# Kernel tuning notes

Hardware: AMD Instinct MI355X
Metric: run time of the kernel (lower is better)

The kernel has to match this reference:

```python
import jax, jax.numpy as jnp
import numpy as np

EPS = 1e-6

def setup_inputs() -> dict:
    key = jax.random.key(0)
    ks = jax.random.split(key, 9)
    B, T, D = 4, 1024, 128
    sc = 1.0 / np.sqrt(D)
    return {
        "x_seq": jax.random.normal(ks[0], (B, T, D), dtype=jnp.float32),
        "Wq": jax.random.uniform(ks[1], (D, D), jnp.float32, -sc, sc),
        "bq": jax.random.uniform(ks[2], (D,), jnp.float32, -sc, sc),
        "Wk": jax.random.uniform(ks[3], (D, D), jnp.float32, -sc, sc),
        "bk": jax.random.uniform(ks[4], (D,), jnp.float32, -sc, sc),
        "Wv": jax.random.uniform(ks[5], (D, D), jnp.float32, -sc, sc),
        "bv": jax.random.uniform(ks[6], (D,), jnp.float32, -sc, sc),
        "Wa": jax.random.uniform(ks[7], (D, D), jnp.float32, -sc, sc),
        "ba": jax.random.uniform(ks[8], (D,), jnp.float32, -sc, sc),
    }

def reference(x_seq, Wq, bq, Wk, bk, Wv, bv, Wa, ba):
    B, T, D = x_seq.shape
    q = jax.nn.relu(x_seq @ Wq.T + bq)          # [B,T,D]
    k = jax.nn.relu(x_seq @ Wk.T + bk)
    v = x_seq @ Wv.T + bv
    A = jax.nn.sigmoid(x_seq @ Wa.T + ba)       # per-step decay gate

    def step(carry, inp):
        s, z = carry                             # s:[B,D,D], z:[B,D]
        a_t, k_t, v_t, q_t = inp                 # each [B,D]
        s = a_t[:, :, None] * s + k_t[:, :, None] * v_t[:, None, :]  # s[b,i,j]=a_i*s + k_i v_j
        z = a_t * z + k_t
        num = jnp.einsum('bi,bij->bj', q_t, s)
        den = jnp.sum(q_t * z, axis=-1, keepdims=True) + EPS
        return (s, z), num / den

    s0 = jnp.zeros((B, D, D), x_seq.dtype)
    z0 = jnp.zeros((B, D), x_seq.dtype)
    xs = (jnp.swapaxes(A, 0, 1), jnp.swapaxes(k, 0, 1),
          jnp.swapaxes(v, 0, 1), jnp.swapaxes(q, 0, 1))  # time-major [T,B,D]
    _, y = jax.lax.scan(step, (s0, z0), xs)
    return jnp.swapaxes(y, 0, 1)                 # [B,T,D]
```

## Files before the change

kernel.cpp:

```cpp
#include <hip/hip_runtime.h>

#define BB 4
#define TT 1024
#define DD 128
#define LL 32
#define CC 32
#define EPSV 1e-6f

#define BTD (BB*TT*DD)
#define BCD (BB*CC*DD)

#define OFF_QC   0
#define OFF_KH   (OFF_QC + BTD)
#define OFF_V    (OFF_KH + BTD)
#define OFF_G    (OFF_V  + BTD)
#define OFF_CL   (OFF_G  + BTD)
#define OFF_KS   (OFF_CL + BCD)
#define OFF_Z0   (OFF_KS + BCD)
#define OFF_U    (OFF_Z0 + BCD)
#define OFF_S0   (OFF_U  + BB*CC*DD*DD)

__global__ __launch_bounds__(256) void k_gemm(
    const float* __restrict__ x,
    const float* __restrict__ Wq, const float* __restrict__ bq,
    const float* __restrict__ Wk, const float* __restrict__ bk,
    const float* __restrict__ Wv, const float* __restrict__ bv,
    const float* __restrict__ Wa, const float* __restrict__ ba,
    float* __restrict__ ws)
{
    __shared__ float xs [64][DD];
    __shared__ float wsh[64][132];

    const int tid = threadIdx.x;
    const int bx  = blockIdx.x;
    const int rt  = bx >> 3;
    const int mt  = bx & 7;
    const int m   = mt >> 1;
    const int jh  = mt & 1;

    const float* W    = (m==0)?Wq : (m==1)?Wk : (m==2)?Wv : Wa;
    const float* bias = (m==0)?bq : (m==1)?bk : (m==2)?bv : ba;

    {
        const float4* xg = (const float4*)(x + (size_t)rt*64*DD);
        const float4* wg = (const float4*)(W + (size_t)jh*64*DD);
        #pragma unroll
        for (int r=0;r<8;r++){
            int f = tid + r*256;
            *(float4*)&xs [f>>5][(f&31)*4] = xg[f];
            *(float4*)&wsh[f>>5][(f&31)*4] = wg[f];
        }
    }
    __syncthreads();

    const int ci = tid & 15;
    const int ri = tid >> 4;

    float acc[4][4];
    #pragma unroll
    for (int cc=0;cc<4;cc++){
        float bv_ = bias[jh*64 + ci + 16*cc];
        #pragma unroll
        for (int rr=0;rr<4;rr++) acc[rr][cc]=bv_;
    }

    #pragma unroll 2
    for (int k4=0; k4<32; k4++){
        float4 xa0 = *(const float4*)&xs[ri     ][k4*4];
        float4 xa1 = *(const float4*)&xs[ri + 16][k4*4];
        float4 xa2 = *(const float4*)&xs[ri + 32][k4*4];
        float4 xa3 = *(const float4*)&xs[ri + 48][k4*4];
        #pragma unroll
        for (int cc=0;cc<4;cc++){
            float4 w = *(const float4*)&wsh[ci+16*cc][k4*4];
            acc[0][cc] = fmaf(xa0.x,w.x, fmaf(xa0.y,w.y, fmaf(xa0.z,w.z, fmaf(xa0.w,w.w, acc[0][cc]))));
            acc[1][cc] = fmaf(xa1.x,w.x, fmaf(xa1.y,w.y, fmaf(xa1.z,w.z, fmaf(xa1.w,w.w, acc[1][cc]))));
            acc[2][cc] = fmaf(xa2.x,w.x, fmaf(xa2.y,w.y, fmaf(xa2.z,w.z, fmaf(xa2.w,w.w, acc[2][cc]))));
            acc[3][cc] = fmaf(xa3.x,w.x, fmaf(xa3.y,w.y, fmaf(xa3.z,w.z, fmaf(xa3.w,w.w, acc[3][cc]))));
        }
    }

    float* dst = ws + ((m==0)?OFF_QC : (m==1)?OFF_KH : (m==2)?OFF_V : OFF_G);
    #pragma unroll
    for (int rr=0;rr<4;rr++){
        int row = rt*64 + ri + 16*rr;
        #pragma unroll
        for (int cc=0;cc<4;cc++){
            float v = acc[rr][cc];
            if (m==0 || m==1) v = fmaxf(v, 0.f);
            else if (m==3)    v = 1.f/(1.f+__expf(-v));
            dst[(size_t)row*DD + jh*64 + ci + 16*cc] = v;
        }
    }
}

__global__ __launch_bounds__(256) void k_chunk(float* __restrict__ ws)
{
    __shared__ float qs [LL][32];
    __shared__ float krs[LL][32];
    __shared__ float gs [LL][32];
    __shared__ float vs [LL][DD];
    __shared__ float kbs[LL][32];

    const int tid = threadIdx.x;
    const int bq_ = blockIdx.x;
    const int bc  = bq_ >> 2;
    const int iq  = bq_ & 3;
    const int ibase = iq*32;
    const int b   = bc / CC;
    const int t0  = (bc % CC) * LL;
    const size_t tile = (size_t)(b*TT + t0)*DD;

    {
        const int t = tid >> 3, c4 = (tid & 7)*4;
        const size_t off = tile + (size_t)t*DD + ibase + c4;
        *(float4*)&qs [t][c4] = *(const float4*)(ws + OFF_QC + off);
        *(float4*)&krs[t][c4] = *(const float4*)(ws + OFF_KH + off);
        *(float4*)&gs [t][c4] = *(const float4*)(ws + OFF_G  + off);
        #pragma unroll
        for (int r=0;r<4;r++){
            int f = tid + r*256;
            int tv = f >> 5, cv = (f & 31)*4;
            *(float4*)&vs[tv][cv] = *(const float4*)(ws + OFF_V + tile + (size_t)tv*DD + cv);
        }
    }
    __syncthreads();

    if (tid < 32){
        float c = 1.f;
        #pragma unroll
        for (int t=0;t<LL;t++){ c *= gs[t][tid]; gs[t][tid] = c; }
        ws[OFF_CL + (size_t)bc*DD + ibase + tid] = c;
    }
    __syncthreads();

    {
        const int col = tid & 31;
        const int tg  = tid >> 5;
        const float cl = gs[LL-1][col];
        #pragma unroll
        for (int r=0;r<4;r++){
            int t = tg*4 + r;
            float cv = gs[t][col];
            ws[OFF_QC + tile + (size_t)t*DD + ibase + col] = qs[t][col] * cv;
            float kh = krs[t][col] / cv;
            ws[OFF_KH + tile + (size_t)t*DD + ibase + col] = kh;
            kbs[t][col] = kh * cl;
        }
    }
    __syncthreads();

    if (tid < 32){
        float s = 0.f;
        #pragma unroll
        for (int t=0;t<LL;t++) s += kbs[t][tid];
        ws[OFF_KS + (size_t)bc*DD + ibase + tid] = s;
    }

    const int j  = tid & 127;
    const int ih = tid >> 7;
    float vr[LL];
    #pragma unroll
    for (int u=0;u<LL;u++) vr[u]=vs[u][j];
    float* Ug = ws + OFF_U + (size_t)bc*DD*DD;
    #pragma unroll
    for (int i4=0;i4<4;i4++){
        int il = ih*16 + i4*4;
        float a0=0.f,a1=0.f,a2=0.f,a3=0.f;
        #pragma unroll
        for (int u=0;u<LL;u++){
            float4 kb4 = *(const float4*)(&kbs[u][il]);
            float vu = vr[u];
            a0 = fmaf(kb4.x,vu,a0); a1 = fmaf(kb4.y,vu,a1);
            a2 = fmaf(kb4.z,vu,a2); a3 = fmaf(kb4.w,vu,a3);
        }
        Ug[(size_t)(ibase+il+0)*DD + j]=a0; Ug[(size_t)(ibase+il+1)*DD + j]=a1;
        Ug[(size_t)(ibase+il+2)*DD + j]=a2; Ug[(size_t)(ibase+il+3)*DD + j]=a3;
    }
}

__global__ __launch_bounds__(128) void k_scan(float* __restrict__ ws)
{
    __shared__ float cls[CC], kss[CC];
    const int bi = blockIdx.x;
    const int b  = bi >> 7;
    const int i  = bi & 127;
    const int j  = threadIdx.x;

    if (j < CC)        cls[j]      = ws[OFF_CL + (size_t)(b*CC + j)*DD + i];
    else if (j < 2*CC) kss[j - CC] = ws[OFF_KS + (size_t)(b*CC + j - CC)*DD + i];
    __syncthreads();

    const float* U  = ws + OFF_U;
    float*       s0 = ws + OFF_S0;
    float*       z0 = ws + OFF_Z0;
    const size_t base = (size_t)b*CC*DD*DD + (size_t)i*DD + j;

    float up[16];
    #pragma unroll
    for (int p=0;p<16;p++) up[p] = U[base + (size_t)p*DD*DD];

    float s = 0.f, z = 0.f;
    #pragma unroll
    for (int ch=0; ch<CC; ch++){
        s0[base + (size_t)ch*DD*DD] = s;
        if (j==0) z0[(size_t)(b*CC+ch)*DD + i] = z;
        float u  = up[ch & 15];
        if (ch + 16 < CC) up[ch & 15] = U[base + (size_t)(ch+16)*DD*DD];
        float cl = cls[ch];
        s = fmaf(cl, s, u);
        z = fmaf(cl, z, kss[ch]);
    }
}

__global__ __launch_bounds__(256) void k_out(const float* __restrict__ ws, float* __restrict__ y)
{
    __shared__ float khs[LL][DD+4];
    __shared__ float qcs[16][DD+4];
    __shared__ float vsm[LL][68];
    __shared__ float s0s[32][68];
    __shared__ float Ss[16][LL];
    __shared__ float denS[16];
    __shared__ float z0s[DD];

    const int tid = threadIdx.x;
    const int blk = blockIdx.x;
    const int bc  = blk >> 2;
    const int th  = (blk >> 1) & 1;
    const int jh  = blk & 1;
    const int tbase = th * 16;
    const int jbase = jh * 64;
    const int b   = bc / CC;
    const int ch  = bc % CC;
    const int t0  = ch * LL;
    const size_t tile = (size_t)(b*TT + t0)*DD;
    const float* s0g = ws + OFF_S0 + (size_t)bc*DD*DD;

    {
        const float4* khg = (const float4*)(ws + OFF_KH + tile);
        #pragma unroll
        for (int r=0;r<4;r++){
            int f = tid + r*256;
            int t = f >> 5, k4 = f & 31;
            *(float4*)&khs[t][k4*4] = khg[f];
        }
        const float4* qcg = (const float4*)(ws + OFF_QC + tile + (size_t)tbase*DD);
        #pragma unroll
        for (int r=0;r<2;r++){
            int f = tid + r*256;
            int t = f >> 5, k4 = f & 31;
            *(float4*)&qcs[t][k4*4] = qcg[f];
        }
        #pragma unroll
        for (int r=0;r<2;r++){
            int f = tid + r*256;
            int t = f >> 4, c = (f & 15)*4;
            *(float4*)&vsm[t][c] =
                *(const float4*)(ws + OFF_V + tile + (size_t)t*DD + jbase + c);
        }
        if (tid < DD) z0s[tid] = ws[OFF_Z0 + (size_t)bc*DD + tid];
    }
    __syncthreads();

    {
        const int tl = tid >> 4;
        const int tg = tbase + tl;
        #pragma unroll
        for (int uu=0; uu<2; uu++){
            int u = (tid & 15)*2 + uu;
            float s = 0.f;
            #pragma unroll 8
            for (int k4=0; k4<32; k4++){
                float4 q4 = *(const float4*)&qcs[tl][k4*4];
                float4 h4 = *(const float4*)&khs[u][k4*4];
                s = fmaf(q4.x,h4.x, fmaf(q4.y,h4.y, fmaf(q4.z,h4.z, fmaf(q4.w,h4.w, s))));
            }
            Ss[tl][u] = (u <= tg) ? s : 0.f;
        }
    }
    __syncthreads();

    if (tid < 16){
        int tl = tid;
        float d = EPSV;
        #pragma unroll
        for (int u=0; u<LL; u++) d += Ss[tl][u];
        #pragma unroll 8
        for (int kk=0; kk<DD; kk++) d += qcs[tl][kk]*z0s[kk];
        denS[tl] = d;
    }

    const int tl = tid >> 4;
    const int j0 = (tid & 15) * 4;
    float y4[4] = {0.f,0.f,0.f,0.f};

    __syncthreads();
    #pragma unroll 8
    for (int u=0; u<LL; u++){
        float sv = Ss[tl][u];
        float4 v4 = *(const float4*)&vsm[u][j0];
        y4[0]=fmaf(sv,v4.x,y4[0]); y4[1]=fmaf(sv,v4.y,y4[1]);
        y4[2]=fmaf(sv,v4.z,y4[2]); y4[3]=fmaf(sv,v4.w,y4[3]);
    }

    for (int sl=0; sl<4; sl++){
        __syncthreads();
        #pragma unroll
        for (int r=0;r<2;r++){
            int f = tid + r*256;
            int row = f >> 4, c4 = (f & 15)*4;
            *(float4*)&s0s[row][c4] =
                *(const float4*)(s0g + (size_t)(sl*32 + row)*DD + jbase + c4);
        }
        __syncthreads();
        #pragma unroll 8
        for (int ii=0; ii<32; ii++){
            float qv = qcs[tl][sl*32+ii];
            float4 s4 = *(const float4*)&s0s[ii][j0];
            y4[0]=fmaf(qv,s4.x,y4[0]); y4[1]=fmaf(qv,s4.y,y4[1]);
            y4[2]=fmaf(qv,s4.z,y4[2]); y4[3]=fmaf(qv,s4.w,y4[3]);
        }
    }

    const float rd = 1.f/denS[tl];
    float* yg = y + tile + (size_t)(tbase + tl)*DD + jbase + j0;
    *(float4*)yg = make_float4(y4[0]*rd, y4[1]*rd, y4[2]*rd, y4[3]*rd);
}

extern "C" void kernel_launch(void* const* d_in, const int* in_sizes, int n_in,
                              void* d_out, int out_size, void* d_ws, size_t ws_size,
                              hipStream_t stream)
{
    const float* x  = (const float*)d_in[0];
    const float* Wq = (const float*)d_in[1]; const float* bq = (const float*)d_in[2];
    const float* Wk = (const float*)d_in[3]; const float* bk = (const float*)d_in[4];
    const float* Wv = (const float*)d_in[5]; const float* bv = (const float*)d_in[6];
    const float* Wa = (const float*)d_in[7]; const float* ba = (const float*)d_in[8];
    float* ws = (float*)d_ws;
    float* yo = (float*)d_out;

    hipLaunchKernelGGL(k_gemm,  dim3(512),     dim3(256), 0, stream,
                       x, Wq,bq, Wk,bk, Wv,bv, Wa,ba, ws);
    hipLaunchKernelGGL(k_chunk, dim3(BB*CC*4), dim3(256), 0, stream, ws);
    hipLaunchKernelGGL(k_scan,  dim3(BB*DD),   dim3(128), 0, stream, ws);
    hipLaunchKernelGGL(k_out,   dim3(BB*CC*4), dim3(256), 0, stream, ws, yo);
}
```

Baseline: 113.6 us.

## Widen k_out blocks to full D columns and register-prefetch S0 slices

k_out now uses 512-thread blocks that each cover all 128 output columns for 16 timesteps, instead of splitting columns across two blocks. This removes the duplicated loads of kh/qc and the duplicated QK^T score computation that the column split caused. It also prefetches the next 32-row slice of the S0 state into registers while the current slice is consumed from shared memory, overlapping global loads with compute. In exchange the grid is halved to 256 blocks and each block needs more shared memory and registers, which lowers parallelism and occupancy.

Measured after the change: 137.8 us. +21.3%, slower.

```diff
diff --git a/kernel.cpp b/kernel.cpp
--- a/kernel.cpp
+++ b/kernel.cpp
@@ -213,70 +213,65 @@
     }
 }
 
-__global__ __launch_bounds__(256) void k_out(const float* __restrict__ ws, float* __restrict__ y)
+__global__ __launch_bounds__(512) void k_out(const float* __restrict__ ws, float* __restrict__ y)
 {
     __shared__ float khs[LL][DD+4];
     __shared__ float qcs[16][DD+4];
-    __shared__ float vsm[LL][68];
-    __shared__ float s0s[32][68];
+    __shared__ float vsm[LL][DD+4];
+    __shared__ float s0s[32][DD+4];
     __shared__ float Ss[16][LL];
     __shared__ float denS[16];
     __shared__ float z0s[DD];
 
     const int tid = threadIdx.x;
     const int blk = blockIdx.x;
-    const int bc  = blk >> 2;
-    const int th  = (blk >> 1) & 1;
-    const int jh  = blk & 1;
+    const int bc  = blk >> 1;
+    const int th  = blk & 1;
     const int tbase = th * 16;
-    const int jbase = jh * 64;
     const int b   = bc / CC;
     const int ch  = bc % CC;
     const int t0  = ch * LL;
     const size_t tile = (size_t)(b*TT + t0)*DD;
     const float* s0g = ws + OFF_S0 + (size_t)bc*DD*DD;
 
+    float4 pre[2];
     {
         const float4* khg = (const float4*)(ws + OFF_KH + tile);
-        #pragma unroll
-        for (int r=0;r<4;r++){
-            int f = tid + r*256;
+        const float4* vg  = (const float4*)(ws + OFF_V  + tile);
+        #pragma unroll
+        for (int r=0;r<2;r++){
+            int f = tid + r*512;
             int t = f >> 5, k4 = f & 31;
             *(float4*)&khs[t][k4*4] = khg[f];
-        }
-        const float4* qcg = (const float4*)(ws + OFF_QC + tile + (size_t)tbase*DD);
+            *(float4*)&vsm[t][k4*4] = vg [f];
+        }
+        if (tid < 512){
+            int f = tid;
+            int t = f >> 5, k4 = f & 31;
+            const float4* qcg = (const float4*)(ws + OFF_QC + tile + (size_t)tbase*DD);
+            *(float4*)&qcs[t][k4*4] = qcg[f];
+        }
+        if (tid < DD) z0s[tid] = ws[OFF_Z0 + (size_t)bc*DD + tid];
         #pragma unroll
         for (int r=0;r<2;r++){
-            int f = tid + r*256;
-            int t = f >> 5, k4 = f & 31;
-            *(float4*)&qcs[t][k4*4] = qcg[f];
-        }
-        #pragma unroll
-        for (int r=0;r<2;r++){
-            int f = tid + r*256;
-            int t = f >> 4, c = (f & 15)*4;
-            *(float4*)&vsm[t][c] =
-                *(const float4*)(ws + OFF_V + tile + (size_t)t*DD + jbase + c);
-        }
-        if (tid < DD) z0s[tid] = ws[OFF_Z0 + (size_t)bc*DD + tid];
-    }
-    __syncthreads();
-
-    {
-        const int tl = tid >> 4;
+            int f = tid + r*512;
+            pre[r] = ((const float4*)s0g)[f];
+        }
+    }
+    __syncthreads();
+
+    {
+        const int tl = tid >> 5;
+        const int u  = tid & 31;
         const int tg = tbase + tl;
-        #pragma unroll
-        for (int uu=0; uu<2; uu++){
-            int u = (tid & 15)*2 + uu;
-            float s = 0.f;
-            #pragma unroll 8
-            for (int k4=0; k4<32; k4++){
-                float4 q4 = *(const float4*)&qcs[tl][k4*4];
-                float4 h4 = *(const float4*)&khs[u][k4*4];
-                s = fmaf(q4.x,h4.x, fmaf(q4.y,h4.y, fmaf(q4.z,h4.z, fmaf(q4.w,h4.w, s))));
-            }
-            Ss[tl][u] = (u <= tg) ? s : 0.f;
-        }
+        float s = 0.f;
+        #pragma unroll 8
+        for (int k4=0; k4<32; k4++){
+            float4 q4 = *(const float4*)&qcs[tl][k4*4];
+            float4 h4 = *(const float4*)&khs[u][k4*4];
+            s = fmaf(q4.x,h4.x, fmaf(q4.y,h4.y, fmaf(q4.z,h4.z, fmaf(q4.w,h4.w, s))));
+        }
+        Ss[tl][u] = (u <= tg) ? s : 0.f;
     }
     __syncthreads();
 
@@ -290,8 +285,8 @@
         denS[tl] = d;
     }
 
-    const int tl = tid >> 4;
-    const int j0 = (tid & 15) * 4;
+    const int tl = tid >> 5;
+    const int j0 = (tid & 31) * 4;
     float y4[4] = {0.f,0.f,0.f,0.f};
 
     __syncthreads();
@@ -307,10 +302,13 @@
         __syncthreads();
         #pragma unroll
         for (int r=0;r<2;r++){
-            int f = tid + r*256;
-            int row = f >> 4, c4 = (f & 15)*4;
-            *(float4*)&s0s[row][c4] =
-                *(const float4*)(s0g + (size_t)(sl*32 + row)*DD + jbase + c4);
+            int f = tid + r*512;
+            *(float4*)&s0s[f>>5][(f&31)*4] = pre[r];
+        }
+        if (sl < 3){
+            const float4* sg = (const float4*)(s0g + (size_t)(sl+1)*32*DD);
+            #pragma unroll
+            for (int r=0;r<2;r++) pre[r] = sg[tid + r*512];
         }
         __syncthreads();
         #pragma unroll 8
@@ -323,7 +321,7 @@
     }
 
     const float rd = 1.f/denS[tl];
-    float* yg = y + tile + (size_t)(tbase + tl)*DD + jbase + j0;
+    float* yg = y + tile + (size_t)(tbase + tl)*DD + j0;
     *(float4*)yg = make_float4(y4[0]*rd, y4[1]*rd, y4[2]*rd, y4[3]*rd);
 }
 
@@ -343,5 +341,5 @@
                        x, Wq,bq, Wk,bk, Wv,bv, Wa,ba, ws);
     hipLaunchKernelGGL(k_chunk, dim3(BB*CC*4), dim3(256), 0, stream, ws);
     hipLaunchKernelGGL(k_scan,  dim3(BB*DD),   dim3(128), 0, stream, ws);
-    hipLaunchKernelGGL(k_out,   dim3(BB*CC*4), dim3(256), 0, stream, ws, yo);
-}
+    hipLaunchKernelGGL(k_out,   dim3(BB*CC*2), dim3(512), 0, stream, ws, yo);
+}
```
